# Kernel tuning notes

Measured on AMD Instinct MI355X. Metric: run time of the kernel, lower is better.

## Reference

```python
import jax, jax.numpy as jnp
import numpy as np

B, S, D, H = 2, 2048, 1024, 16
DK = D // H


def setup_inputs() -> dict:
    key = jax.random.key(0)
    ks = jax.random.split(key, 10)
    scale = 1.0 / np.sqrt(D)
    x = jax.random.normal(ks[0], (B, S, D), dtype=jnp.float32)
    # causal mask: 1 = attend, 0 = masked (module's create_causal_mask)
    mask = jnp.tril(jnp.ones((S, S), dtype=jnp.int32))[None, None]
    Wq = jax.random.normal(ks[1], (D, D), jnp.float32) * scale
    bq = jax.random.normal(ks[2], (D,), jnp.float32) * 0.01
    Wk = jax.random.normal(ks[3], (D, D), jnp.float32) * scale
    bk = jax.random.normal(ks[4], (D,), jnp.float32) * 0.01
    Wv = jax.random.normal(ks[5], (D, D), jnp.float32) * scale
    bv = jax.random.normal(ks[6], (D,), jnp.float32) * 0.01
    Wo = jax.random.normal(ks[7], (D, D), jnp.float32) * scale
    bo = jax.random.normal(ks[8], (D,), jnp.float32) * 0.01
    return {"x": x, "mask": mask, "Wq": Wq, "bq": bq, "Wk": Wk, "bk": bk,
            "Wv": Wv, "bv": bv, "Wo": Wo, "bo": bo}


def reference(x, mask, Wq, bq, Wk, bk, Wv, bv, Wo, bo):
    b, s, _ = x.shape
    # projections; [B,S,D] -> [B,H,S,DK]
    def split_heads(t):
        return t.reshape(b, s, H, DK).transpose(0, 2, 1, 3)
    Q = split_heads(x @ Wq + bq)
    K = split_heads(x @ Wk + bk)
    V = split_heads(x @ Wv + bv)
    scores = jnp.einsum('bhqd,bhkd->bhqk', Q, K) / np.sqrt(DK)
    scores = jnp.where(mask == 0, jnp.float32(-1e9), scores)
    attn = jax.nn.softmax(scores, axis=-1)  # dropout p=0 -> identity
    ctx = jnp.einsum('bhqk,bhkd->bhqd', attn, V)
    ctx = ctx.transpose(0, 2, 1, 3).reshape(b, s, D)
    return ctx @ Wo + bo
```

## Files before the change

kernel.cpp:

```cpp
#include <hip/hip_runtime.h>
#include <hip/hip_bf16.h>


typedef _Float16 f16x8 __attribute__((ext_vector_type(8)));
typedef _Float16 f16x4 __attribute__((ext_vector_type(4)));
typedef float f32x4 __attribute__((ext_vector_type(4)));

#define QSCALE 0.180336880111112f

__device__ __forceinline__ void async_copy16(const _Float16* gsrc,
                                             _Float16* ldst) {
  __builtin_amdgcn_global_load_lds(
      (const __attribute__((address_space(1))) void*)gsrc,
      (__attribute__((address_space(3))) void*)ldst, 16, 0, 0);
}

__global__ __launch_bounds__(256) void prep(
    const float* __restrict__ x, _Float16* __restrict__ xh,
    const float* __restrict__ W0, const float* __restrict__ W1,
    const float* __restrict__ W2, const float* __restrict__ W3,
    _Float16* __restrict__ T0, _Float16* __restrict__ T1,
    _Float16* __restrict__ T2, _Float16* __restrict__ T3) {
  if (blockIdx.x < 4096) {
    int i = (blockIdx.x * 256 + threadIdx.x) * 4;
    float4 v = *(const float4*)(x + i);
    f16x4 o;
    o.x = (_Float16)v.x; o.y = (_Float16)v.y;
    o.z = (_Float16)v.z; o.w = (_Float16)v.w;
    *(f16x4*)(xh + i) = o;
    return;
  }
  const int id = blockIdx.x - 4096;
  const int w = id >> 10, rem = id & 1023;
  const int bx = rem & 31, by = rem >> 5;
  const float* W; _Float16* T;
  switch (w) {
    case 0: W = W0; T = T0; break;
    case 1: W = W1; T = T1; break;
    case 2: W = W2; T = T2; break;
    default: W = W3; T = T3; break;
  }
  __shared__ _Float16 tile[32][33];
  const int tx = threadIdx.x & 31, ty = threadIdx.x >> 5;
  const int n0 = bx * 32, k0 = by * 32;
  for (int i = 0; i < 4; i++) {
    int kk = k0 + ty + i * 8;
    tile[ty + i * 8][tx] = (_Float16)W[(size_t)kk * 1024 + n0 + tx];
  }
  __syncthreads();
  for (int i = 0; i < 4; i++) {
    int nn = n0 + ty + i * 8;
    T[(size_t)nn * 1024 + k0 + tx] = tile[tx][ty + i * 8];
  }
}

__global__ __launch_bounds__(256) void gemm_qkv(
    const _Float16* __restrict__ A, const _Float16* __restrict__ BtAll,
    const float* __restrict__ bq, const float* __restrict__ bk,
    const float* __restrict__ bv, _Float16* __restrict__ Qh,
    _Float16* __restrict__ Kh, _Float16* __restrict__ VT) {
  __shared__ _Float16 As[128 * 32];
  __shared__ _Float16 Bs[128 * 32];
  const int tid = threadIdx.x;
  const int wave = tid >> 6, lane = tid & 63;
  const int lr = lane & 15, lq = lane >> 4;
  const int m0 = blockIdx.x * 128, n0 = blockIdx.y * 128;
  const int rw = (wave & 1) * 64, cw = (wave >> 1) * 64;

  const int sel = blockIdx.y >> 3;
  const float* bias = sel == 0 ? bq : (sel == 1 ? bk : bv);
  const int c0 = n0 & 1023;

  f32x4 acc[4][4] = {};
  const int r0 = wave * 32 + (lane >> 2);
  const int woff = (lane & 3) * 8;

  for (int kt = 0; kt < 1024; kt += 32) {
    __syncthreads();
    async_copy16(A + (size_t)(m0 + r0) * 1024 + kt + woff, As + r0 * 32 + woff);
    async_copy16(A + (size_t)(m0 + r0 + 16) * 1024 + kt + woff,
                 As + (r0 + 16) * 32 + woff);
    async_copy16(BtAll + (size_t)(n0 + r0) * 1024 + kt + woff,
                 Bs + r0 * 32 + woff);
    async_copy16(BtAll + (size_t)(n0 + r0 + 16) * 1024 + kt + woff,
                 Bs + (r0 + 16) * 32 + woff);
    __syncthreads();
    f16x8 af[4], bf[4];
    for (int i = 0; i < 4; i++)
      af[i] = *(const f16x8*)(As + (rw + i * 16 + lr) * 32 + lq * 8);
    for (int j = 0; j < 4; j++)
      bf[j] = *(const f16x8*)(Bs + (cw + j * 16 + lr) * 32 + lq * 8);
    for (int i = 0; i < 4; i++)
      for (int j = 0; j < 4; j++)
        acc[i][j] = __builtin_amdgcn_mfma_f32_16x16x32_f16(af[i], bf[j],
                                                           acc[i][j], 0, 0, 0);
  }

  if (sel == 2) {
    for (int i = 0; i < 4; i++) {
      const int row = m0 + rw + i * 16 + lq * 4;
      const int bb = row >> 11, ss = row & 2047;
      for (int j = 0; j < 4; j++) {
        const int col = c0 + cw + j * 16 + lr;
        const int hh = col >> 6, dk = col & 63;
        const float bvl = bias[col];
        f16x4 pv;
        for (int r = 0; r < 4; r++) pv[r] = (_Float16)(acc[i][j][r] + bvl);
        *(f16x4*)(VT + ((size_t)(bb * 16 + hh) * 64 + dk) * 2048 + ss) = pv;
      }
    }
  } else {
    _Float16* out = sel == 0 ? Qh : Kh;
    const float scl = sel == 0 ? QSCALE : 1.0f;
    for (int i = 0; i < 4; i++) {
      const int row = m0 + rw + i * 16 + lq * 4;
      for (int j = 0; j < 4; j++) {
        const int col = c0 + cw + j * 16 + lr;
        const float bvl = bias[col];
        for (int r = 0; r < 4; r++)
          out[(size_t)(row + r) * 1024 + col] =
              (_Float16)((acc[i][j][r] + bvl) * scl);
      }
    }
  }
}

__global__ __launch_bounds__(256) void gemm_out(
    const _Float16* __restrict__ A, const _Float16* __restrict__ Bt,
    const float* __restrict__ bias, float* __restrict__ out) {
  __shared__ _Float16 As[128 * 32];
  __shared__ _Float16 Bs[128 * 32];
  const int tid = threadIdx.x;
  const int wave = tid >> 6, lane = tid & 63;
  const int lr = lane & 15, lq = lane >> 4;
  const int m0 = blockIdx.x * 128, n0 = blockIdx.y * 128;
  const int rw = (wave & 1) * 64, cw = (wave >> 1) * 64;
  f32x4 acc[4][4] = {};
  const int r0 = wave * 32 + (lane >> 2);
  const int woff = (lane & 3) * 8;

  for (int kt = 0; kt < 1024; kt += 32) {
    __syncthreads();
    async_copy16(A + (size_t)(m0 + r0) * 1024 + kt + woff, As + r0 * 32 + woff);
    async_copy16(A + (size_t)(m0 + r0 + 16) * 1024 + kt + woff,
                 As + (r0 + 16) * 32 + woff);
    async_copy16(Bt + (size_t)(n0 + r0) * 1024 + kt + woff,
                 Bs + r0 * 32 + woff);
    async_copy16(Bt + (size_t)(n0 + r0 + 16) * 1024 + kt + woff,
                 Bs + (r0 + 16) * 32 + woff);
    __syncthreads();
    f16x8 af[4], bf[4];
    for (int i = 0; i < 4; i++)
      af[i] = *(const f16x8*)(As + (rw + i * 16 + lr) * 32 + lq * 8);
    for (int j = 0; j < 4; j++)
      bf[j] = *(const f16x8*)(Bs + (cw + j * 16 + lr) * 32 + lq * 8);
    for (int i = 0; i < 4; i++)
      for (int j = 0; j < 4; j++)
        acc[i][j] = __builtin_amdgcn_mfma_f32_16x16x32_f16(af[i], bf[j],
                                                           acc[i][j], 0, 0, 0);
  }
  for (int i = 0; i < 4; i++) {
    const int row = m0 + rw + i * 16 + lq * 4;
    for (int j = 0; j < 4; j++) {
      const int col = n0 + cw + j * 16 + lr;
      const float bvl = bias[col];
      for (int r = 0; r < 4; r++)
        out[(size_t)(row + r) * 1024 + col] = acc[i][j][r] + bvl;
    }
  }
}

__global__ __launch_bounds__(512) void attn(const _Float16* __restrict__ Q,
                                            const _Float16* __restrict__ K,
                                            const _Float16* __restrict__ VT,
                                            _Float16* __restrict__ ctx) {
  const int qt = 15 - blockIdx.x;
  const int h = blockIdx.y, b = blockIdx.z;
  const int tid = threadIdx.x, wave = tid >> 6, lane = tid & 63;
  const int lr = lane & 15, lq = lane >> 4;
  const int q0 = qt * 128;
  const int qmin = q0 + wave * 16;
  const size_t qkbase = ((size_t)b * 2048) * 1024 + h * 64;
  const size_t vtbase = ((size_t)(b * 16 + h)) * 64 * 2048;

  __shared__ _Float16 Ks[2][64 * 72];
  __shared__ _Float16 Vs[2][64 * 72];

  const _Float16* qp = Q + qkbase + (size_t)(qmin + lr) * 1024 + lq * 8;
  f16x8 qf0 = *(const f16x8*)qp;
  f16x8 qf1 = *(const f16x8*)(qp + 32);

  float mrow = -1e30f, lsum = 0.f;
  f32x4 o[4] = {};

  const int sgr = tid >> 3, sgc = (tid & 7) * 8;
  const _Float16* Kg0 = K + qkbase + (size_t)sgr * 1024 + sgc;
  const _Float16* Vg0 = VT + vtbase + (size_t)sgr * 2048 + sgc;
  uint4 ka = *(const uint4*)Kg0;
  uint4 va = *(const uint4*)Vg0;

  const int tmax = 2 * qt + 1;
  for (int t = 0;; t++) {
    _Float16* ksb = Ks[t & 1];
    _Float16* vsb = Vs[t & 1];
    *(uint4*)(ksb + sgr * 72 + sgc) = ka;
    *(uint4*)(vsb + sgr * 72 + sgc) = va;
    __syncthreads();
    if (t < tmax) {
      ka = *(const uint4*)(Kg0 + (size_t)(t + 1) * 64 * 1024);
      va = *(const uint4*)(Vg0 + (t + 1) * 64);
    }

    const int kv0 = t * 64;
    if (kv0 <= qmin + 15) {
      f32x4 s[4];
      for (int ks = 0; ks < 4; ks++) {
        f16x8 k0 = *(const f16x8*)(ksb + (ks * 16 + lr) * 72 + lq * 8);
        f16x8 k1 = *(const f16x8*)(ksb + (ks * 16 + lr) * 72 + 32 + lq * 8);
        f32x4 z = {};
        z = __builtin_amdgcn_mfma_f32_16x16x32_f16(k0, qf0, z, 0, 0, 0);
        z = __builtin_amdgcn_mfma_f32_16x16x32_f16(k1, qf1, z, 0, 0, 0);
        s[ks] = z;
      }
      if (kv0 + 63 > qmin) {
        const int qcol = qmin + lr;
        for (int ks = 0; ks < 4; ks++)
          for (int r = 0; r < 4; r++)
            if (kv0 + ks * 16 + lq * 4 + r > qcol) s[ks][r] = -1e30f;
      }
      float mx = s[0][0];
      for (int ks = 0; ks < 4; ks++)
        for (int r = 0; r < 4; r++) mx = fmaxf(mx, s[ks][r]);
      mx = fmaxf(mx, __shfl_xor(mx, 16));
      mx = fmaxf(mx, __shfl_xor(mx, 32));
      float mnew = fmaxf(mrow, mx);
      float alpha = exp2f(mrow - mnew);
      mrow = mnew;
      float rs = 0.f;
      f16x4 pa[4];
      for (int ks = 0; ks < 4; ks++)
        for (int r = 0; r < 4; r++) {
          float p = exp2f(s[ks][r] - mnew);
          rs += p;
          pa[ks][r] = (_Float16)p;
        }
      rs += __shfl_xor(rs, 16);
      rs += __shfl_xor(rs, 32);
      lsum = lsum * alpha + rs;
      if (__any(alpha != 1.0f)) {
        float ar[4];
        for (int r = 0; r < 4; r++) ar[r] = __shfl(alpha, lq * 4 + r);
        for (int dn = 0; dn < 4; dn++)
          for (int r = 0; r < 4; r++) o[dn][r] *= ar[r];
      }
      for (int ks = 0; ks < 4; ks++)
        for (int dn = 0; dn < 4; dn++) {
          f16x4 vf =
              *(const f16x4*)(vsb + (dn * 16 + lr) * 72 + ks * 16 + lq * 4);
          o[dn] =
              __builtin_amdgcn_mfma_f32_16x16x16f16(pa[ks], vf, o[dn], 0, 0, 0);
        }
    }
    if (t == tmax) break;
  }

  for (int r = 0; r < 4; r++) {
    float lv = __shfl(lsum, lq * 4 + r);
    float inv = 1.0f / lv;
    const int row = qmin + lq * 4 + r;
    for (int dn = 0; dn < 4; dn++)
      ctx[qkbase + (size_t)row * 1024 + dn * 16 + lr] =
          (_Float16)(o[dn][r] * inv);
  }
}

extern "C" void kernel_launch(void* const* d_in, const int* in_sizes, int n_in,
                              void* d_out, int out_size, void* d_ws,
                              size_t ws_size, hipStream_t stream) {
  const float* x  = (const float*)d_in[0];
  const float* Wq = (const float*)d_in[2];
  const float* bq = (const float*)d_in[3];
  const float* Wk = (const float*)d_in[4];
  const float* bk = (const float*)d_in[5];
  const float* Wv = (const float*)d_in[6];
  const float* bv = (const float*)d_in[7];
  const float* Wo = (const float*)d_in[8];
  const float* bo = (const float*)d_in[9];
  float* out = (float*)d_out;

  char* ws = (char*)d_ws;
  const size_t MB = 1 << 20;
  _Float16* xh  = (_Float16*)(ws);
  _Float16* WTs = (_Float16*)(ws + 8 * MB);
  _Float16* WqT = WTs;
  _Float16* WkT = (_Float16*)(ws + 10 * MB);
  _Float16* WvT = (_Float16*)(ws + 12 * MB);
  _Float16* WoT = (_Float16*)(ws + 14 * MB);
  _Float16* Qh  = (_Float16*)(ws + 16 * MB);
  _Float16* Kh  = (_Float16*)(ws + 24 * MB);
  _Float16* VT  = (_Float16*)(ws + 32 * MB);
  _Float16* ctx = (_Float16*)(ws);

  prep<<<8192, 256, 0, stream>>>(x, xh, Wq, Wk, Wv, Wo, WqT, WkT, WvT, WoT);
  gemm_qkv<<<dim3(32, 24), 256, 0, stream>>>(xh, WTs, bq, bk, bv, Qh, Kh, VT);
  attn<<<dim3(16, 16, 2), 512, 0, stream>>>(Qh, Kh, VT, ctx);
  gemm_out<<<dim3(32, 8), 256, 0, stream>>>(ctx, WoT, bo, out);
}
```

Before: 234.3 us.

## Shrink attention query tile to 64 and gemm_out N-tile to 64 for more blocks

The attention kernel now uses 64-query tiles with 4 waves (256 threads) instead of 128-query tiles with 8 waves. Each block loads only the KV tiles up to its diagonal, which removes the idle waves and skipped tiles of the old causal schedule and doubles the block count. The output GEMM tile narrows from 128x128 to 128x64, giving 512 blocks for better occupancy across CUs at the cost of re-reading A more often. P is also packed to fp16 with a round-toward-zero pack instead of per-element casts, a small rounding difference.

```diff
diff --git a/kernel.cpp b/kernel.cpp
--- a/kernel.cpp
+++ b/kernel.cpp
@@ -4,6 +4,7 @@
 
 typedef _Float16 f16x8 __attribute__((ext_vector_type(8)));
 typedef _Float16 f16x4 __attribute__((ext_vector_type(4)));
+typedef _Float16 f16x2 __attribute__((ext_vector_type(2)));
 typedef float f32x4 __attribute__((ext_vector_type(4)));
 
 #define QSCALE 0.180336880111112f
@@ -129,14 +130,15 @@
     const _Float16* __restrict__ A, const _Float16* __restrict__ Bt,
     const float* __restrict__ bias, float* __restrict__ out) {
   __shared__ _Float16 As[128 * 32];
-  __shared__ _Float16 Bs[128 * 32];
+  __shared__ _Float16 Bs[64 * 32];
   const int tid = threadIdx.x;
   const int wave = tid >> 6, lane = tid & 63;
   const int lr = lane & 15, lq = lane >> 4;
-  const int m0 = blockIdx.x * 128, n0 = blockIdx.y * 128;
-  const int rw = (wave & 1) * 64, cw = (wave >> 1) * 64;
-  f32x4 acc[4][4] = {};
+  const int m0 = blockIdx.x * 128, n0 = blockIdx.y * 64;
+  const int rw = (wave & 1) * 64, cw = (wave >> 1) * 32;
+  f32x4 acc[4][2] = {};
   const int r0 = wave * 32 + (lane >> 2);
+  const int br = tid >> 2;
   const int woff = (lane & 3) * 8;
 
   for (int kt = 0; kt < 1024; kt += 32) {
@@ -144,24 +146,22 @@
     async_copy16(A + (size_t)(m0 + r0) * 1024 + kt + woff, As + r0 * 32 + woff);
     async_copy16(A + (size_t)(m0 + r0 + 16) * 1024 + kt + woff,
                  As + (r0 + 16) * 32 + woff);
-    async_copy16(Bt + (size_t)(n0 + r0) * 1024 + kt + woff,
-                 Bs + r0 * 32 + woff);
-    async_copy16(Bt + (size_t)(n0 + r0 + 16) * 1024 + kt + woff,
-                 Bs + (r0 + 16) * 32 + woff);
-    __syncthreads();
-    f16x8 af[4], bf[4];
+    async_copy16(Bt + (size_t)(n0 + br) * 1024 + kt + woff,
+                 Bs + br * 32 + woff);
+    __syncthreads();
+    f16x8 af[4], bf[2];
     for (int i = 0; i < 4; i++)
       af[i] = *(const f16x8*)(As + (rw + i * 16 + lr) * 32 + lq * 8);
-    for (int j = 0; j < 4; j++)
+    for (int j = 0; j < 2; j++)
       bf[j] = *(const f16x8*)(Bs + (cw + j * 16 + lr) * 32 + lq * 8);
     for (int i = 0; i < 4; i++)
-      for (int j = 0; j < 4; j++)
+      for (int j = 0; j < 2; j++)
         acc[i][j] = __builtin_amdgcn_mfma_f32_16x16x32_f16(af[i], bf[j],
                                                            acc[i][j], 0, 0, 0);
   }
   for (int i = 0; i < 4; i++) {
     const int row = m0 + rw + i * 16 + lq * 4;
-    for (int j = 0; j < 4; j++) {
+    for (int j = 0; j < 2; j++) {
       const int col = n0 + cw + j * 16 + lr;
       const float bvl = bias[col];
       for (int r = 0; r < 4; r++)
@@ -170,18 +170,18 @@
   }
 }
 
-__global__ __launch_bounds__(512) void attn(const _Float16* __restrict__ Q,
+__global__ __launch_bounds__(256) void attn(const _Float16* __restrict__ Q,
                                             const _Float16* __restrict__ K,
                                             const _Float16* __restrict__ VT,
                                             _Float16* __restrict__ ctx) {
-  const int qt = 15 - blockIdx.x;
-  const int h = blockIdx.y, b = blockIdx.z;
+  const int qt = 31 - blockIdx.y;
+  const int bh = blockIdx.x;
+  const int b = bh >> 4, h = bh & 15;
   const int tid = threadIdx.x, wave = tid >> 6, lane = tid & 63;
   const int lr = lane & 15, lq = lane >> 4;
-  const int q0 = qt * 128;
-  const int qmin = q0 + wave * 16;
+  const int qmin = qt * 64 + wave * 16;
   const size_t qkbase = ((size_t)b * 2048) * 1024 + h * 64;
-  const size_t vtbase = ((size_t)(b * 16 + h)) * 64 * 2048;
+  const size_t vtbase = ((size_t)bh) * 64 * 2048;
 
   __shared__ _Float16 Ks[2][64 * 72];
   __shared__ _Float16 Vs[2][64 * 72];
@@ -193,75 +193,79 @@
   float mrow = -1e30f, lsum = 0.f;
   f32x4 o[4] = {};
 
-  const int sgr = tid >> 3, sgc = (tid & 7) * 8;
+  const int sgr = tid >> 2, sgc = (tid & 3) * 8;
   const _Float16* Kg0 = K + qkbase + (size_t)sgr * 1024 + sgc;
   const _Float16* Vg0 = VT + vtbase + (size_t)sgr * 2048 + sgc;
-  uint4 ka = *(const uint4*)Kg0;
-  uint4 va = *(const uint4*)Vg0;
-
-  const int tmax = 2 * qt + 1;
-  for (int t = 0;; t++) {
+  uint4 ka = *(const uint4*)Kg0, kb = *(const uint4*)(Kg0 + 32);
+  uint4 va = *(const uint4*)Vg0, vb = *(const uint4*)(Vg0 + 32);
+
+  for (int t = 0; t <= qt; t++) {
     _Float16* ksb = Ks[t & 1];
     _Float16* vsb = Vs[t & 1];
     *(uint4*)(ksb + sgr * 72 + sgc) = ka;
+    *(uint4*)(ksb + sgr * 72 + sgc + 32) = kb;
     *(uint4*)(vsb + sgr * 72 + sgc) = va;
-    __syncthreads();
-    if (t < tmax) {
-      ka = *(const uint4*)(Kg0 + (size_t)(t + 1) * 64 * 1024);
-      va = *(const uint4*)(Vg0 + (t + 1) * 64);
+    *(uint4*)(vsb + sgr * 72 + sgc + 32) = vb;
+    __syncthreads();
+    if (t < qt) {
+      const _Float16* kg = Kg0 + (size_t)(t + 1) * 64 * 1024;
+      const _Float16* vg = Vg0 + (t + 1) * 64;
+      ka = *(const uint4*)kg; kb = *(const uint4*)(kg + 32);
+      va = *(const uint4*)vg; vb = *(const uint4*)(vg + 32);
     }
 
     const int kv0 = t * 64;
-    if (kv0 <= qmin + 15) {
-      f32x4 s[4];
-      for (int ks = 0; ks < 4; ks++) {
-        f16x8 k0 = *(const f16x8*)(ksb + (ks * 16 + lr) * 72 + lq * 8);
-        f16x8 k1 = *(const f16x8*)(ksb + (ks * 16 + lr) * 72 + 32 + lq * 8);
-        f32x4 z = {};
-        z = __builtin_amdgcn_mfma_f32_16x16x32_f16(k0, qf0, z, 0, 0, 0);
-        z = __builtin_amdgcn_mfma_f32_16x16x32_f16(k1, qf1, z, 0, 0, 0);
-        s[ks] = z;
+    f32x4 s[4];
+    for (int ks = 0; ks < 4; ks++) {
+      f16x8 k0 = *(const f16x8*)(ksb + (ks * 16 + lr) * 72 + lq * 8);
+      f16x8 k1 = *(const f16x8*)(ksb + (ks * 16 + lr) * 72 + 32 + lq * 8);
+      f32x4 z = {};
+      z = __builtin_amdgcn_mfma_f32_16x16x32_f16(k0, qf0, z, 0, 0, 0);
+      z = __builtin_amdgcn_mfma_f32_16x16x32_f16(k1, qf1, z, 0, 0, 0);
+      s[ks] = z;
+    }
+    if (t == qt) {
+      const int qcol = qmin + lr;
+      for (int ks = 0; ks < 4; ks++)
+        for (int r = 0; r < 4; r++)
+          if (kv0 + ks * 16 + lq * 4 + r > qcol) s[ks][r] = -1e30f;
+    }
+    float mx = s[0][0];
+    for (int ks = 0; ks < 4; ks++)
+      for (int r = 0; r < 4; r++) mx = fmaxf(mx, s[ks][r]);
+    mx = fmaxf(mx, __shfl_xor(mx, 16));
+    mx = fmaxf(mx, __shfl_xor(mx, 32));
+    float mnew = fmaxf(mrow, mx);
+    float alpha = exp2f(mrow - mnew);
+    mrow = mnew;
+    float rs = 0.f;
+    f16x4 pa[4];
+    for (int ks = 0; ks < 4; ks++) {
+      float p0 = exp2f(s[ks][0] - mnew);
+      float p1 = exp2f(s[ks][1] - mnew);
+      float p2 = exp2f(s[ks][2] - mnew);
+      float p3 = exp2f(s[ks][3] - mnew);
+      rs += (p0 + p1) + (p2 + p3);
+      f16x2 q01 = __builtin_bit_cast(f16x2, __builtin_amdgcn_cvt_pkrtz(p0, p1));
+      f16x2 q23 = __builtin_bit_cast(f16x2, __builtin_amdgcn_cvt_pkrtz(p2, p3));
+      pa[ks] = __builtin_shufflevector(q01, q23, 0, 1, 2, 3);
+    }
+    rs += __shfl_xor(rs, 16);
+    rs += __shfl_xor(rs, 32);
+    lsum = lsum * alpha + rs;
+    if (__any(alpha != 1.0f)) {
+      float ar[4];
+      for (int r = 0; r < 4; r++) ar[r] = __shfl(alpha, lq * 4 + r);
+      for (int dn = 0; dn < 4; dn++)
+        for (int r = 0; r < 4; r++) o[dn][r] *= ar[r];
+    }
+    for (int ks = 0; ks < 4; ks++)
+      for (int dn = 0; dn < 4; dn++) {
+        f16x4 vf =
+            *(const f16x4*)(vsb + (dn * 16 + lr) * 72 + ks * 16 + lq * 4);
+        o[dn] =
+            __builtin_amdgcn_mfma_f32_16x16x16f16(pa[ks], vf, o[dn], 0, 0, 0);
       }
-      if (kv0 + 63 > qmin) {
-        const int qcol = qmin + lr;
-        for (int ks = 0; ks < 4; ks++)
-          for (int r = 0; r < 4; r++)
-            if (kv0 + ks * 16 + lq * 4 + r > qcol) s[ks][r] = -1e30f;
-      }
-      float mx = s[0][0];
-      for (int ks = 0; ks < 4; ks++)
-        for (int r = 0; r < 4; r++) mx = fmaxf(mx, s[ks][r]);
-      mx = fmaxf(mx, __shfl_xor(mx, 16));
-      mx = fmaxf(mx, __shfl_xor(mx, 32));
-      float mnew = fmaxf(mrow, mx);
-      float alpha = exp2f(mrow - mnew);
-      mrow = mnew;
-      float rs = 0.f;
-      f16x4 pa[4];
-      for (int ks = 0; ks < 4; ks++)
-        for (int r = 0; r < 4; r++) {
-          float p = exp2f(s[ks][r] - mnew);
-          rs += p;
-          pa[ks][r] = (_Float16)p;
-        }
-      rs += __shfl_xor(rs, 16);
-      rs += __shfl_xor(rs, 32);
-      lsum = lsum * alpha + rs;
-      if (__any(alpha != 1.0f)) {
-        float ar[4];
-        for (int r = 0; r < 4; r++) ar[r] = __shfl(alpha, lq * 4 + r);
-        for (int dn = 0; dn < 4; dn++)
-          for (int r = 0; r < 4; r++) o[dn][r] *= ar[r];
-      }
-      for (int ks = 0; ks < 4; ks++)
-        for (int dn = 0; dn < 4; dn++) {
-          f16x4 vf =
-              *(const f16x4*)(vsb + (dn * 16 + lr) * 72 + ks * 16 + lq * 4);
-          o[dn] =
-              __builtin_amdgcn_mfma_f32_16x16x16f16(pa[ks], vf, o[dn], 0, 0, 0);
-        }
-    }
-    if (t == tmax) break;
   }
 
   for (int r = 0; r < 4; r++) {
@@ -303,6 +307,6 @@
 
   prep<<<8192, 256, 0, stream>>>(x, xh, Wq, Wk, Wv, Wo, WqT, WkT, WvT, WoT);
   gemm_qkv<<<dim3(32, 24), 256, 0, stream>>>(xh, WTs, bq, bk, bv, Qh, Kh, VT);
-  attn<<<dim3(16, 16, 2), 512, 0, stream>>>(Qh, Kh, VT, ctx);
-  gemm_out<<<dim3(32, 8), 256, 0, stream>>>(ctx, WoT, bo, out);
-}
+  attn<<<dim3(32, 32), 256, 0, stream>>>(Qh, Kh, VT, ctx);
+  gemm_out<<<dim3(32, 16), 256, 0, stream>>>(ctx, WoT, bo, out);
+}
```

After: 200.3 us. 1.17x faster.
